# Kernel tuning notes

Hardware: AMD Instinct MI355X
Metric: run time of the kernel (lower is better)

## Reference

```python
import jax, jax.numpy as jnp
import numpy as np

B, N, D_IN, D_OUT, H, E = 16, 512, 256, 256, 8, 131072
HD = D_OUT // H  # 32


def setup_inputs() -> dict:
    key = jax.random.key(0)
    ks = jax.random.split(key, 12)
    h = jax.random.normal(ks[0], (B, N, D_IN), dtype=jnp.float32)
    # global edge indices; dst constrained to same graph as src
    src = jax.random.randint(ks[1], (E,), 0, B * N, dtype=jnp.int64 if jax.config.jax_enable_x64 else jnp.int32)
    dst = (src // N) * N + jax.random.randint(ks[2], (E,), 0, N, dtype=src.dtype)
    s_in = 1.0 / np.sqrt(D_IN)
    s_out = 1.0 / np.sqrt(D_OUT)
    Wq = jax.random.normal(ks[3], (D_IN, D_OUT), jnp.float32) * s_in
    bq = jnp.zeros((D_OUT,), jnp.float32)
    Wk = jax.random.normal(ks[4], (D_IN, D_OUT), jnp.float32) * s_in
    bk = jnp.zeros((D_OUT,), jnp.float32)
    Wv = jax.random.normal(ks[5], (D_IN, D_OUT), jnp.float32) * s_in
    bv = jnp.zeros((D_OUT,), jnp.float32)
    Wo = jax.random.normal(ks[6], (D_OUT, D_OUT), jnp.float32) * s_out
    bo = jnp.zeros((D_OUT,), jnp.float32)
    return dict(h=h, src=src, dst=dst, Wq=Wq, bq=bq, Wk=Wk, bk=bk, Wv=Wv, bv=bv, Wo=Wo, bo=bo)


def reference(h, src, dst, Wq, bq, Wk, bk, Wv, bv, Wo, bo):
    scale = 1.0 / np.sqrt(HD)
    # projections -> (B, H, N, HD)
    q = (h @ Wq + bq).reshape(B, N, H, HD).transpose(0, 2, 1, 3)
    k = (h @ Wk + bk).reshape(B, N, H, HD).transpose(0, 2, 1, 3)
    v = (h @ Wv + bv).reshape(B, N, H, HD).transpose(0, 2, 1, 3)
    scores = jnp.einsum('bhqd,bhkd->bhqk', q, k) * scale  # (B,H,N,N)
    # build per-graph edge mask by scatter (replaces torch python loop)
    b = src // N
    r = src % N
    c = dst % N
    mask = jnp.zeros((B, N, N), dtype=bool).at[b, r, c].set(True)
    mask = mask | jnp.eye(N, dtype=bool)[None]  # self-loops
    scores = jnp.where(mask[:, None], scores, jnp.float32(-1e9))
    w = jax.nn.softmax(scores, axis=-1)
    out = jnp.einsum('bhqk,bhkd->bhqd', w, v)
    out = out.transpose(0, 2, 1, 3).reshape(B, N, D_OUT)
    out = out @ Wo + bo
    return out.reshape(-1, D_OUT)  # (B*N, D_OUT)
```

## Files before the change

### kernel.cpp

```cpp
#include <hip/hip_runtime.h>
#include <hip/hip_bf16.h>

#define BB 16
#define NN 512
#define DIN 256
#define DOUT 256
#define HH 8
#define HD 32
#define EE 131072
#define MM (BB*NN)
#define BH (BB*HH)

typedef unsigned short ushort_t;
typedef __attribute__((ext_vector_type(8))) short bf16x8;
typedef __attribute__((ext_vector_type(4))) float f32x4;

__device__ __forceinline__ unsigned short f2bf(float f) {
    unsigned int u = __float_as_uint(f);
    unsigned int r = (u + 0x7fffu + ((u >> 16) & 1u)) >> 16;
    return (unsigned short)r;
}

__device__ __forceinline__ void gload16(const ushort_t* g, ushort_t* l) {
    __builtin_amdgcn_global_load_lds((__attribute__((address_space(1))) void*)(void*)g,
                                     (__attribute__((address_space(3))) void*)l, 16, 0, 0);
}

__device__ __forceinline__ void ld16bf(const ushort_t* p, float* f) {
    uint4 u0 = *(const uint4*)p;
    uint4 u1 = *(const uint4*)(p + 8);
    unsigned int w[8] = {u0.x, u0.y, u0.z, u0.w, u1.x, u1.y, u1.z, u1.w};
    #pragma unroll
    for (int i = 0; i < 8; ++i) {
        f[2 * i]     = __uint_as_float(w[i] << 16);
        f[2 * i + 1] = __uint_as_float(w[i] & 0xffff0000u);
    }
}

__global__ __launch_bounds__(256) void prep(
    const float* __restrict__ h,
    const float* __restrict__ Wq, const float* __restrict__ Wk,
    const float* __restrict__ Wv, const float* __restrict__ Wo,
    unsigned int* __restrict__ mask, ushort_t* __restrict__ hb,
    ushort_t* __restrict__ Wt, ushort_t* __restrict__ Wot) {
    const int bid = blockIdx.x;
    const int t = threadIdx.x;
    if (bid < 128) {
        uint4 z = {0u, 0u, 0u, 0u};
        ((uint4*)mask)[bid * 256 + t] = z;
    } else if (bid < 1152) {
        int chunk = (bid - 128) * 256 + t;
        float4 a = *(const float4*)(h + (size_t)chunk * 8);
        float4 b = *(const float4*)(h + (size_t)chunk * 8 + 4);
        ushort_t o[8] = {f2bf(a.x), f2bf(a.y), f2bf(a.z), f2bf(a.w),
                         f2bf(b.x), f2bf(b.y), f2bf(b.z), f2bf(b.w)};
        *(uint4*)(hb + (size_t)chunk * 8) = *(const uint4*)o;
    } else {
        int tg = (bid - 1152) * 256 + t;
        int n = tg >> 8, k = tg & 255;
        if (n < 768) {
            const float* W = (n < 256) ? Wq : (n < 512) ? Wk : Wv;
            Wt[(size_t)n * 256 + k] = f2bf(W[(size_t)k * 256 + (n & 255)]);
        } else {
            int nn = n - 768;
            Wot[(size_t)nn * 256 + k] = f2bf(Wo[(size_t)k * 256 + nn]);
        }
    }
}

__global__ __launch_bounds__(256) void mask_gemm(
    const int* __restrict__ src, const int* __restrict__ dst, unsigned int* __restrict__ mask,
    const ushort_t* __restrict__ A, const ushort_t* __restrict__ Bt,
    const float* __restrict__ b0, const float* __restrict__ b1, const float* __restrict__ b2,
    ushort_t* __restrict__ qb, ushort_t* __restrict__ kb, ushort_t* __restrict__ vb) {
    __shared__ ushort_t As[128 * 64];
    __shared__ ushort_t Bs[128 * 64];
    const int bid = blockIdx.x;
    const int t = threadIdx.x;

    if (bid >= 384) {
        int tt = (bid - 384) * 256 + t;
        if (tt < EE) {
            int s = src[tt], d = dst[tt];
            int b = s / NN, r = s % NN, c = d % NN;
            atomicOr(&mask[((size_t)(b * NN + r)) * 16 + (c >> 5)], 1u << (c & 31));
        }
        if (tt < MM) {
            atomicOr(&mask[(size_t)tt * 16 + ((tt & 511) >> 5)], 1u << (tt & 31));
        }
        return;
    }

    const int xcd = bid & 7, idx = bid >> 3;
    const int m0 = (xcd * 8 + (idx & 7)) * 128;
    const int n0 = (idx >> 3) * 128;
    const int wid = t >> 6, lane = t & 63, g = lane >> 4, c = lane & 15;
    const int wr = wid >> 1, wc = wid & 1;
    const int c7 = c & 7;

    f32x4 acc[4][4];
    #pragma unroll
    for (int mi = 0; mi < 4; ++mi)
        #pragma unroll
        for (int nj = 0; nj < 4; ++nj) acc[mi][nj] = (f32x4){0.f, 0.f, 0.f, 0.f};

    #define STAGE_QKV(kt) { \
        const int k0s = (kt) * 64; \
        _Pragma("unroll") \
        for (int i = 0; i < 4; ++i) { \
            int p = i * 256 + t; \
            int row = p >> 3, ss = (p & 7) ^ (row & 7); \
            int ldoff = (i * 256 + wid * 64) * 8; \
            gload16(A  + (size_t)(m0 + row) * 256 + k0s + ss * 8, &As[ldoff]); \
            gload16(Bt + (size_t)(n0 + row) * 256 + k0s + ss * 8, &Bs[ldoff]); \
        } \
    }

    STAGE_QKV(0);
    __syncthreads();
    for (int kt = 0; kt < 4; ++kt) {
        #pragma unroll
        for (int kk = 0; kk < 2; ++kk) {
            bf16x8 av[4], bv4[4];
            #pragma unroll
            for (int mi = 0; mi < 4; ++mi) {
                int row = wr * 64 + mi * 16 + c;
                av[mi] = *(const bf16x8*)&As[row * 64 + (((kk * 4 + g) ^ c7) << 3)];
            }
            #pragma unroll
            for (int nj = 0; nj < 4; ++nj) {
                int row = wc * 64 + nj * 16 + c;
                bv4[nj] = *(const bf16x8*)&Bs[row * 64 + (((kk * 4 + g) ^ c7) << 3)];
            }
            #pragma unroll
            for (int mi = 0; mi < 4; ++mi)
                #pragma unroll
                for (int nj = 0; nj < 4; ++nj)
                    acc[mi][nj] = __builtin_amdgcn_mfma_f32_16x16x32_bf16(av[mi], bv4[nj], acc[mi][nj], 0, 0, 0);
        }
        if (kt < 3) {
            __syncthreads();
            STAGE_QKV(kt + 1);
            __syncthreads();
        }
    }

    #pragma unroll
    for (int mi = 0; mi < 4; ++mi) {
        #pragma unroll
        for (int nj = 0; nj < 4; ++nj) {
            const f32x4 av = acc[mi][nj];
            const int m_base = m0 + wr * 64 + mi * 16 + 4 * g;
            const int n_base = n0 + wc * 64 + nj * 16;
            const int z = n_base >> 8, nn = n_base & 255;
            const int hh = nn >> 5, hd = (nn & 31) + c;
            const float* bp = (z == 0) ? b0 : (z == 1) ? b1 : b2;
            const float bias = bp[nn + c];
            const int b = m_base >> 9, nrow = m_base & 511;
            ushort_t* dst2 = (z == 0) ? qb : (z == 1) ? kb : vb;
            #pragma unroll
            for (int r = 0; r < 4; ++r)
                dst2[(((size_t)(b * 8 + hh)) * 512 + nrow + r) * 32 + hd] = f2bf(av[r] + bias);
        }
    }
}

__global__ __launch_bounds__(256) void attn_sparse3(
    const ushort_t* __restrict__ qb, const ushort_t* __restrict__ kb,
    const ushort_t* __restrict__ vb, const unsigned int* __restrict__ mask,
    ushort_t* __restrict__ attnb) {
    __shared__ ushort_t colsS[4][64];
    const int wid = threadIdx.x >> 6, lane = threadIdx.x & 63;
    const int xcd = blockIdx.x & 7, j = blockIdx.x >> 3;
    const int b = xcd * 2 + (j >> 7);
    const int q = (j & 127) * 4 + wid;
    const int row = b * 512 + q;
    const int e2 = lane >> 4, h = (lane >> 1) & 7, half = lane & 1;
    const float SCALE = 0.17677669529663687f;

    unsigned int word = (lane < 16) ? mask[(size_t)row * 16 + lane] : 0u;
    int pc = __popc(word);
    int pre = pc;
    #pragma unroll
    for (int o = 1; o < 16; o <<= 1) {
        int v = __shfl_up(pre, o);
        if ((lane & 15) >= o) pre += v;
    }
    int off = pre - pc;
    while (word) {
        int bit = __ffs(word) - 1;
        word &= word - 1;
        if (off < 64) colsS[wid][off] = (ushort_t)(lane * 32 + bit);
        ++off;
    }
    int cnt = __shfl(pre, 15);
    cnt = cnt < 64 ? cnt : 64;

    const size_t hb_base = ((size_t)(b * 8 + h)) * 512;
    const int d0 = half * 16;
    float qf[16];
    ld16bf(qb + (hb_base + q) * 32 + d0, qf);

    float acc[16];
    #pragma unroll
    for (int d = 0; d < 16; ++d) acc[d] = 0.f;
    float l = 0.f;

    #pragma unroll 2
    for (int e = 0; e < cnt; e += 4) {
        int slot = e + e2;
        int col = colsS[wid][slot < cnt ? slot : 0];
        const ushort_t* kp = kb + (hb_base + col) * 32 + d0;
        const ushort_t* vp = vb + (hb_base + col) * 32 + d0;
        float kf[16], vf[16];
        ld16bf(kp, kf);
        ld16bf(vp, vf);
        float s0 = 0.f, s1 = 0.f;
        #pragma unroll
        for (int d = 0; d < 8; ++d) {
            s0 = fmaf(qf[d], kf[d], s0);
            s1 = fmaf(qf[8 + d], kf[8 + d], s1);
        }
        float s = s0 + s1;
        s += __shfl_xor(s, 1);
        float p = (slot < cnt) ? __expf(fmaf(s, SCALE, -16.0f)) : 0.f;
        l += p;
        #pragma unroll
        for (int d = 0; d < 16; ++d) acc[d] = fmaf(p, vf[d], acc[d]);
    }

    #pragma unroll
    for (int d = 0; d < 16; ++d) {
        acc[d] += __shfl_xor(acc[d], 16);
        acc[d] += __shfl_xor(acc[d], 32);
    }
    l += __shfl_xor(l, 16);
    l += __shfl_xor(l, 32);

    if (e2 == 0) {
        float rl = 1.0f / l;
        ushort_t o[16];
        #pragma unroll
        for (int d = 0; d < 16; ++d) o[d] = f2bf(acc[d] * rl);
        ushort_t* op = attnb + (size_t)row * 256 + h * 32 + d0;
        *(uint4*)op       = *(const uint4*)o;
        *(uint4*)(op + 8) = *(const uint4*)(o + 8);
    }
}

__global__ __launch_bounds__(256) void gemm_out(
    const ushort_t* __restrict__ A, const ushort_t* __restrict__ Bt,
    const float* __restrict__ b0, float* __restrict__ fout) {
    __shared__ ushort_t As[64 * 64];
    __shared__ ushort_t Bs[64 * 64];
    const int t = threadIdx.x;
    const int m0 = blockIdx.x * 64, n0 = blockIdx.y * 64;
    const int wid = t >> 6, lane = t & 63, g = lane >> 4, c = lane & 15;
    const int wr = wid >> 1, wc = wid & 1;
    const int c7 = c & 7;

    f32x4 acc00 = {0.f,0.f,0.f,0.f}, acc01 = acc00, acc10 = acc00, acc11 = acc00;

    #define STAGE_OUT(kt) { \
        const int k0s = (kt) * 64; \
        _Pragma("unroll") \
        for (int i = 0; i < 2; ++i) { \
            int p = i * 256 + t; \
            int row = p >> 3, ss = (p & 7) ^ (row & 7); \
            int ldoff = (i * 256 + wid * 64) * 8; \
            gload16(A  + (size_t)(m0 + row) * 256 + k0s + ss * 8, &As[ldoff]); \
            gload16(Bt + (size_t)(n0 + row) * 256 + k0s + ss * 8, &Bs[ldoff]); \
        } \
    }

    STAGE_OUT(0);
    __syncthreads();
    for (int kt = 0; kt < 4; ++kt) {
        #pragma unroll
        for (int kk = 0; kk < 2; ++kk) {
            int sw = ((kk * 4 + g) ^ c7) << 3;
            bf16x8 a0 = *(const bf16x8*)&As[(wr * 32 + c) * 64 + sw];
            bf16x8 a1 = *(const bf16x8*)&As[(wr * 32 + 16 + c) * 64 + sw];
            bf16x8 bb0 = *(const bf16x8*)&Bs[(wc * 32 + c) * 64 + sw];
            bf16x8 bb1 = *(const bf16x8*)&Bs[(wc * 32 + 16 + c) * 64 + sw];
            acc00 = __builtin_amdgcn_mfma_f32_16x16x32_bf16(a0, bb0, acc00, 0, 0, 0);
            acc01 = __builtin_amdgcn_mfma_f32_16x16x32_bf16(a0, bb1, acc01, 0, 0, 0);
            acc10 = __builtin_amdgcn_mfma_f32_16x16x32_bf16(a1, bb0, acc10, 0, 0, 0);
            acc11 = __builtin_amdgcn_mfma_f32_16x16x32_bf16(a1, bb1, acc11, 0, 0, 0);
        }
        if (kt < 3) {
            __syncthreads();
            STAGE_OUT(kt + 1);
            __syncthreads();
        }
    }

    #pragma unroll
    for (int mi = 0; mi < 2; ++mi) {
        #pragma unroll
        for (int nj = 0; nj < 2; ++nj) {
            const f32x4 av = (mi == 0) ? (nj == 0 ? acc00 : acc01) : (nj == 0 ? acc10 : acc11);
            const int m_base = m0 + wr * 32 + mi * 16 + 4 * g;
            const int n_base = n0 + wc * 32 + nj * 16;
            const float bias = b0[n_base + c];
            #pragma unroll
            for (int r = 0; r < 4; ++r)
                fout[(size_t)(m_base + r) * 256 + n_base + c] = av[r] + bias;
        }
    }
}

extern "C" void kernel_launch(void* const* d_in, const int* in_sizes, int n_in,
                              void* d_out, int out_size, void* d_ws, size_t ws_size,
                              hipStream_t stream) {
    const float* hin = (const float*)d_in[0];
    const int* src   = (const int*)d_in[1];
    const int* dst   = (const int*)d_in[2];
    const float* Wq  = (const float*)d_in[3];
    const float* bq  = (const float*)d_in[4];
    const float* Wk  = (const float*)d_in[5];
    const float* bk  = (const float*)d_in[6];
    const float* Wv  = (const float*)d_in[7];
    const float* bv  = (const float*)d_in[8];
    const float* Wo  = (const float*)d_in[9];
    const float* bo  = (const float*)d_in[10];

    char* ws = (char*)d_ws;
    unsigned int* mask = (unsigned int*)ws;
    ushort_t* hb    = (ushort_t*)(ws + 2129920);
    ushort_t* qb    = (ushort_t*)(ws + 6324224);
    ushort_t* kb    = (ushort_t*)(ws + 10518528);
    ushort_t* vb    = (ushort_t*)(ws + 14712832);
    ushort_t* attnb = (ushort_t*)(ws + 18907136);
    ushort_t* Wt    = (ushort_t*)(ws + 23101440);
    ushort_t* Wot   = (ushort_t*)(ws + 23494656);
    float* out = (float*)d_out;

    prep<<<2176, 256, 0, stream>>>(hin, Wq, Wk, Wv, Wo, mask, hb, Wt, Wot);
    mask_gemm<<<896, 256, 0, stream>>>(src, dst, mask, hb, Wt, bq, bk, bv, qb, kb, vb);
    attn_sparse3<<<2048, 256, 0, stream>>>(qb, kb, vb, mask, attnb);
    gemm_out<<<dim3(MM / 64, 256 / 64), 256, 0, stream>>>(attnb, Wot, bo, out);
}
```

Baseline: 43.51 us.

## Tile weight transpose through LDS and double K-tile depth in GEMMs

```diff
diff --git a/kernel.cpp b/kernel.cpp
--- a/kernel.cpp
+++ b/kernel.cpp
@@ -43,6 +43,7 @@
     const float* __restrict__ Wv, const float* __restrict__ Wo,
     unsigned int* __restrict__ mask, ushort_t* __restrict__ hb,
     ushort_t* __restrict__ Wt, ushort_t* __restrict__ Wot) {
+    __shared__ float ts[64][65];
     const int bid = blockIdx.x;
     const int t = threadIdx.x;
     if (bid < 128) {
@@ -56,14 +57,26 @@
                          f2bf(b.x), f2bf(b.y), f2bf(b.z), f2bf(b.w)};
         *(uint4*)(hb + (size_t)chunk * 8) = *(const uint4*)o;
     } else {
-        int tg = (bid - 1152) * 256 + t;
-        int n = tg >> 8, k = tg & 255;
-        if (n < 768) {
-            const float* W = (n < 256) ? Wq : (n < 512) ? Wk : Wv;
-            Wt[(size_t)n * 256 + k] = f2bf(W[(size_t)k * 256 + (n & 255)]);
-        } else {
-            int nn = n - 768;
-            Wot[(size_t)nn * 256 + k] = f2bf(Wo[(size_t)k * 256 + nn]);
+        const int bid6 = bid - 1152;
+        const int which = bid6 >> 4, tile = bid6 & 15;
+        const int k0 = (tile >> 2) * 64, n0 = (tile & 3) * 64;
+        const float* W = (which == 0) ? Wq : (which == 1) ? Wk : (which == 2) ? Wv : Wo;
+        #pragma unroll
+        for (int i = 0; i < 4; ++i) {
+            int kr = i * 16 + (t >> 4), c4 = (t & 15) * 4;
+            float4 v = *(const float4*)&W[(size_t)(k0 + kr) * 256 + n0 + c4];
+            ts[kr][c4 + 0] = v.x; ts[kr][c4 + 1] = v.y;
+            ts[kr][c4 + 2] = v.z; ts[kr][c4 + 3] = v.w;
+        }
+        __syncthreads();
+        #pragma unroll
+        for (int i = 0; i < 4; ++i) {
+            int nr = i * 16 + (t >> 4), kc = (t & 15) * 4;
+            ushort_t o[4] = {f2bf(ts[kc][nr]), f2bf(ts[kc + 1][nr]),
+                             f2bf(ts[kc + 2][nr]), f2bf(ts[kc + 3][nr])};
+            ushort_t* dstp = (which < 3) ? (Wt + (size_t)(which * 256 + n0 + nr) * 256 + k0 + kc)
+                                         : (Wot + (size_t)(n0 + nr) * 256 + k0 + kc);
+            *(uint2*)dstp = *(const uint2*)o;
         }
     }
 }
@@ -73,8 +86,8 @@
     const ushort_t* __restrict__ A, const ushort_t* __restrict__ Bt,
     const float* __restrict__ b0, const float* __restrict__ b1, const float* __restrict__ b2,
     ushort_t* __restrict__ qb, ushort_t* __restrict__ kb, ushort_t* __restrict__ vb) {
-    __shared__ ushort_t As[128 * 64];
-    __shared__ ushort_t Bs[128 * 64];
+    __shared__ ushort_t As[128 * 128];
+    __shared__ ushort_t Bs[128 * 128];
     const int bid = blockIdx.x;
     const int t = threadIdx.x;
 
@@ -96,7 +109,6 @@
     const int n0 = (idx >> 3) * 128;
     const int wid = t >> 6, lane = t & 63, g = lane >> 4, c = lane & 15;
     const int wr = wid >> 1, wc = wid & 1;
-    const int c7 = c & 7;
 
     f32x4 acc[4][4];
     #pragma unroll
@@ -105,11 +117,11 @@
         for (int nj = 0; nj < 4; ++nj) acc[mi][nj] = (f32x4){0.f, 0.f, 0.f, 0.f};
 
     #define STAGE_QKV(kt) { \
-        const int k0s = (kt) * 64; \
+        const int k0s = (kt) * 128; \
         _Pragma("unroll") \
-        for (int i = 0; i < 4; ++i) { \
+        for (int i = 0; i < 8; ++i) { \
             int p = i * 256 + t; \
-            int row = p >> 3, ss = (p & 7) ^ (row & 7); \
+            int row = p >> 4, ss = (p & 15) ^ (row & 15); \
             int ldoff = (i * 256 + wid * 64) * 8; \
             gload16(A  + (size_t)(m0 + row) * 256 + k0s + ss * 8, &As[ldoff]); \
             gload16(Bt + (size_t)(n0 + row) * 256 + k0s + ss * 8, &Bs[ldoff]); \
@@ -118,19 +130,19 @@
 
     STAGE_QKV(0);
     __syncthreads();
-    for (int kt = 0; kt < 4; ++kt) {
-        #pragma unroll
-        for (int kk = 0; kk < 2; ++kk) {
+    for (int kt = 0; kt < 2; ++kt) {
+        #pragma unroll
+        for (int kk = 0; kk < 4; ++kk) {
             bf16x8 av[4], bv4[4];
             #pragma unroll
             for (int mi = 0; mi < 4; ++mi) {
                 int row = wr * 64 + mi * 16 + c;
-                av[mi] = *(const bf16x8*)&As[row * 64 + (((kk * 4 + g) ^ c7) << 3)];
+                av[mi] = *(const bf16x8*)&As[row * 128 + (((kk * 4 + g) ^ c) << 3)];
             }
             #pragma unroll
             for (int nj = 0; nj < 4; ++nj) {
                 int row = wc * 64 + nj * 16 + c;
-                bv4[nj] = *(const bf16x8*)&Bs[row * 64 + (((kk * 4 + g) ^ c7) << 3)];
+                bv4[nj] = *(const bf16x8*)&Bs[row * 128 + (((kk * 4 + g) ^ c) << 3)];
             }
             #pragma unroll
             for (int mi = 0; mi < 4; ++mi)
@@ -138,9 +150,9 @@
                 for (int nj = 0; nj < 4; ++nj)
                     acc[mi][nj] = __builtin_amdgcn_mfma_f32_16x16x32_bf16(av[mi], bv4[nj], acc[mi][nj], 0, 0, 0);
         }
-        if (kt < 3) {
+        if (kt == 0) {
             __syncthreads();
-            STAGE_QKV(kt + 1);
+            STAGE_QKV(1);
             __syncthreads();
         }
     }
@@ -251,22 +263,21 @@
 __global__ __launch_bounds__(256) void gemm_out(
     const ushort_t* __restrict__ A, const ushort_t* __restrict__ Bt,
     const float* __restrict__ b0, float* __restrict__ fout) {
-    __shared__ ushort_t As[64 * 64];
-    __shared__ ushort_t Bs[64 * 64];
+    __shared__ ushort_t As[64 * 128];
+    __shared__ ushort_t Bs[64 * 128];
     const int t = threadIdx.x;
     const int m0 = blockIdx.x * 64, n0 = blockIdx.y * 64;
     const int wid = t >> 6, lane = t & 63, g = lane >> 4, c = lane & 15;
     const int wr = wid >> 1, wc = wid & 1;
-    const int c7 = c & 7;
 
     f32x4 acc00 = {0.f,0.f,0.f,0.f}, acc01 = acc00, acc10 = acc00, acc11 = acc00;
 
     #define STAGE_OUT(kt) { \
-        const int k0s = (kt) * 64; \
+        const int k0s = (kt) * 128; \
         _Pragma("unroll") \
-        for (int i = 0; i < 2; ++i) { \
+        for (int i = 0; i < 4; ++i) { \
             int p = i * 256 + t; \
-            int row = p >> 3, ss = (p & 7) ^ (row & 7); \
+            int row = p >> 4, ss = (p & 15) ^ (row & 15); \
             int ldoff = (i * 256 + wid * 64) * 8; \
             gload16(A  + (size_t)(m0 + row) * 256 + k0s + ss * 8, &As[ldoff]); \
             gload16(Bt + (size_t)(n0 + row) * 256 + k0s + ss * 8, &Bs[ldoff]); \
@@ -275,22 +286,24 @@
 
     STAGE_OUT(0);
     __syncthreads();
-    for (int kt = 0; kt < 4; ++kt) {
-        #pragma unroll
-        for (int kk = 0; kk < 2; ++kk) {
-            int sw = ((kk * 4 + g) ^ c7) << 3;
-            bf16x8 a0 = *(const bf16x8*)&As[(wr * 32 + c) * 64 + sw];
-            bf16x8 a1 = *(const bf16x8*)&As[(wr * 32 + 16 + c) * 64 + sw];
-            bf16x8 bb0 = *(const bf16x8*)&Bs[(wc * 32 + c) * 64 + sw];
-            bf16x8 bb1 = *(const bf16x8*)&Bs[(wc * 32 + 16 + c) * 64 + sw];
+    for (int kt = 0; kt < 2; ++kt) {
+        #pragma unroll
+        for (int kk = 0; kk < 4; ++kk) {
+            int rowa0 = wr * 32 + c, rowa1 = wr * 32 + 16 + c;
+            int rowb0 = wc * 32 + c, rowb1 = wc * 32 + 16 + c;
+            int sw = ((kk * 4 + g) ^ c) << 3;
+            bf16x8 a0 = *(const bf16x8*)&As[rowa0 * 128 + sw];
+            bf16x8 a1 = *(const bf16x8*)&As[rowa1 * 128 + sw];
+            bf16x8 bb0 = *(const bf16x8*)&Bs[rowb0 * 128 + sw];
+            bf16x8 bb1 = *(const bf16x8*)&Bs[rowb1 * 128 + sw];
             acc00 = __builtin_amdgcn_mfma_f32_16x16x32_bf16(a0, bb0, acc00, 0, 0, 0);
             acc01 = __builtin_amdgcn_mfma_f32_16x16x32_bf16(a0, bb1, acc01, 0, 0, 0);
             acc10 = __builtin_amdgcn_mfma_f32_16x16x32_bf16(a1, bb0, acc10, 0, 0, 0);
             acc11 = __builtin_amdgcn_mfma_f32_16x16x32_bf16(a1, bb1, acc11, 0, 0, 0);
         }
-        if (kt < 3) {
+        if (kt == 0) {
             __syncthreads();
-            STAGE_OUT(kt + 1);
+            STAGE_OUT(1);
             __syncthreads();
         }
     }
@@ -336,7 +349,7 @@
     ushort_t* Wot   = (ushort_t*)(ws + 23494656);
     float* out = (float*)d_out;
 
-    prep<<<2176, 256, 0, stream>>>(hin, Wq, Wk, Wv, Wo, mask, hb, Wt, Wot);
+    prep<<<1216, 256, 0, stream>>>(hin, Wq, Wk, Wv, Wo, mask, hb, Wt, Wot);
     mask_gemm<<<896, 256, 0, stream>>>(src, dst, mask, hb, Wt, bq, bk, bv, qb, kb, vb);
     attn_sparse3<<<2048, 256, 0, stream>>>(qb, kb, vb, mask, attnb);
     gemm_out<<<dim3(MM / 64, 256 / 64), 256, 0, stream>>>(attnb, Wot, bo, out);
```

New measurement: 40.81 us. -6.2%, faster.
